# Kernel tuning notes

Measured on AMD Instinct MI355X. Metric: run time of the kernel, lower is better.

## Reference

```python
import jax, jax.numpy as jnp
import numpy as np

GRID_SIZE = 5
NUM_BASES = 2 ** GRID_SIZE - 1  # 31: actual number of Haar bases produced by the loop

def _haar_edges():
    left, mid, right = [], [], []
    for level in range(GRID_SIZE):
        scale = 2 ** level
        for shift in range(scale):
            left.append(shift / scale)
            mid.append((shift + 0.5) / scale)
            right.append((shift + 1.0) / scale)
    return (np.asarray(left, np.float32), np.asarray(mid, np.float32), np.asarray(right, np.float32))

_LEFT, _MID, _RIGHT = _haar_edges()


def setup_inputs() -> dict:
    key = jax.random.key(0)
    k1, k2, k3 = jax.random.split(key, 3)
    B, IN, OUT = 16384, 256, 256
    x = jax.random.normal(k1, (B, IN), dtype=jnp.float32)
    base_weight = jax.random.normal(k2, (OUT, IN), dtype=jnp.float32) * 0.05
    spline_weight = jax.random.normal(k3, (OUT, IN, NUM_BASES), dtype=jnp.float32) * 0.05
    spline_scaler = jnp.ones((OUT, IN), dtype=jnp.float32)
    return {"x": x, "base_weight": base_weight, "spline_weight": spline_weight, "spline_scaler": spline_scaler}


def reference(x, base_weight, spline_weight, spline_scaler):
    # per-feature min/max normalization over the batch dim
    x_min = jnp.min(x, axis=0, keepdims=True)
    x_max = jnp.max(x, axis=0, keepdims=True)
    xn = (x - x_min) / (x_max - x_min + 1e-8)            # [B, IN]
    left = jnp.asarray(_LEFT, x.dtype)
    mid = jnp.asarray(_MID, x.dtype)
    right = jnp.asarray(_RIGHT, x.dtype)
    xe = xn[..., None]                                    # [B, IN, 1]
    mask1 = ((xe >= left) & (xe < mid)).astype(x.dtype)
    mask2 = ((xe >= mid) & (xe < right)).astype(x.dtype)
    bases = mask1 - mask2                                 # [B, IN, NB]
    base_out = jax.nn.relu(x) @ base_weight.T             # [B, OUT]
    sw = spline_weight * spline_scaler[..., None]         # [OUT, IN, NB]
    wavelet_out = jnp.einsum('bik,oik->bo', bases, sw)    # [B, OUT]
    return base_out + wavelet_out
```

## Files before the change

kernel.cpp:

```cpp
#include <hip/hip_runtime.h>
#include <stdint.h>

typedef short s16x8 __attribute__((ext_vector_type(8)));
typedef float f32x4 __attribute__((ext_vector_type(4)));
typedef unsigned long long u64;

#define IN_F   256
#define OUT_F  256
#define BATCH  16384
#define NB     31
#define KONE   8192
#define KTOT   8448

typedef const __attribute__((address_space(1))) void* as1cvp;
typedef __attribute__((address_space(3))) void* as3vp;

__device__ __forceinline__ unsigned short f2bf(float f) {
    unsigned u = __float_as_uint(f);
    u += 0x7FFFu + ((u >> 16) & 1u);
    return (unsigned short)(u >> 16);
}

__global__ void minmax_part(const float* __restrict__ x,
                            float* __restrict__ pmn, float* __restrict__ pmx) {
    const int t = threadIdx.x;
    const int b0 = blockIdx.x * 32;
    float mn = 3.4e38f, mx = -3.4e38f;
    for (int r = 0; r < 32; ++r) {
        float v = x[(size_t)(b0 + r) * IN_F + t];
        mn = fminf(mn, v);
        mx = fmaxf(mx, v);
    }
    pmn[blockIdx.x * 256 + t] = mn;
    pmx[blockIdx.x * 256 + t] = mx;
}

__global__ __launch_bounds__(64) void minmax_reduce(
    const float* __restrict__ pmn, const float* __restrict__ pmx,
    float* __restrict__ xminF, float* __restrict__ rdenF) {
    const int j = blockIdx.x;
    const int lane = threadIdx.x;
    float mn = 3.4e38f, mx = -3.4e38f;
#pragma unroll
    for (int i = 0; i < 8; ++i) {
        int b = lane * 8 + i;
        mn = fminf(mn, pmn[(size_t)b * 256 + j]);
        mx = fmaxf(mx, pmx[(size_t)b * 256 + j]);
    }
#pragma unroll
    for (int off = 32; off; off >>= 1) {
        mn = fminf(mn, __shfl_down(mn, off));
        mx = fmaxf(mx, __shfl_down(mx, off));
    }
    if (lane == 0) {
        xminF[j] = mn;
        rdenF[j] = 1.0f / (mx - mn + 1e-8f);
    }
}

__global__ __launch_bounds__(256) void build_wb(
    const float* __restrict__ bw, const float* __restrict__ sw,
    const float* __restrict__ sc, unsigned short* __restrict__ Wb) {
    const int o = blockIdx.x, i = threadIdx.x;
    const float s = sc[o * IN_F + i];
    const float* swp = sw + (size_t)(o * IN_F + i) * NB;
    float w[NB];
#pragma unroll
    for (int k = 0; k < NB; ++k) w[k] = swp[k];
    unsigned short* dst = Wb + (size_t)o * KTOT + i * 32;
#pragma unroll
    for (int q = 0; q < 4; ++q) {
        union { s16x8 v; unsigned short s8[8]; } pk;
#pragma unroll
        for (int e = 0; e < 8; ++e) {
            int j = q * 8 + e;
            float acc = 0.f;
#pragma unroll
            for (int l = 0; l < 5; ++l) {
                int kk = (1 << l) - 1 + (j >> (5 - l));
                acc += (((j >> (4 - l)) & 1) ? -w[kk] : w[kk]);
            }
            pk.s8[e] = f2bf(acc * s);
        }
        *(s16x8*)(dst + q * 8) = pk.v;
    }
    Wb[(size_t)o * KTOT + KONE + i] = f2bf(bw[o * IN_F + i]);
}

__global__ __launch_bounds__(256) void leafk(
    const float* __restrict__ x, const float* __restrict__ xminF,
    const float* __restrict__ rdenF, unsigned char* __restrict__ lt) {
    const int lane = threadIdx.x & 63, w = threadIdx.x >> 6;
    const int b0 = blockIdx.x * 64;
    const float4 mn = *(const float4*)(xminF + lane * 4);
    const float4 rd = *(const float4*)(rdenF + lane * 4);
#pragma unroll 4
    for (int r = 0; r < 16; ++r) {
        int row = b0 + w * 16 + r;
        float4 v = *(const float4*)(x + (size_t)row * IN_F + lane * 4);
        unsigned b[4];
        float xs[4] = {v.x, v.y, v.z, v.w};
        float ms[4] = {mn.x, mn.y, mn.z, mn.w};
        float rs[4] = {rd.x, rd.y, rd.z, rd.w};
#pragma unroll
        for (int e = 0; e < 4; ++e) {
            float xn = (xs[e] - ms[e]) * rs[e];
            int l = (int)(xn * 32.0f);
            b[e] = (l >= 0 && l < 32) ? (unsigned)l : 255u;
        }
        unsigned pk = b[0] | (b[1] << 8) | (b[2] << 16) | (b[3] << 24);
        *(unsigned*)(lt + (size_t)row * IN_F + lane * 4) = pk;
    }
}

__global__ __launch_bounds__(256, 4) void gemm_kan(
    const float* __restrict__ x,
    const unsigned short* __restrict__ Wb,
    const unsigned char* __restrict__ lt,
    float* __restrict__ out)
{
    __shared__ unsigned short Bsh[2 * 64 * 64];

    const int t    = threadIdx.x;
    const int lane = t & 63;
    const int wv   = t >> 6;

    const int bid   = blockIdx.x;
    const int sid   = (bid & 7) * 128 + (bid >> 3);
    const int mtile = sid & 127;
    const int ntile = (sid >> 7) & 3;
    const int zz    = sid >> 9;
    const int kbeg  = zz ? 68 : 0;
    const int kend  = zz ? 132 : 68;

    const unsigned char* bbase = (const unsigned char*)(Wb
        + (size_t)(ntile * 64 + wv * 16 + (lane >> 3)) * KTOT
        + (((lane & 7) ^ (lane >> 3)) << 3));

    const int rr = lane & 15, kq = lane >> 4;
    const int r0 = mtile * 128 + wv * 32 + rr;
    const unsigned char* lp0 = lt + (size_t)r0 * IN_F;
    const unsigned char* lp1 = lt + (size_t)(r0 + 16) * IN_F;

    int boff[2][4];
#pragma unroll
    for (int ks = 0; ks < 2; ++ks)
#pragma unroll
        for (int nt = 0; nt < 4; ++nt) {
            int n = nt * 16 + rr, c = ks * 4 + kq;
            boff[ks][nt] = (n << 7) + ((c ^ (n & 7)) << 4);
        }

    {
        const unsigned char* src = bbase + (size_t)kbeg * 128;
        unsigned short* dst = Bsh + (kbeg & 1) * 4096 + wv * 1024;
#pragma unroll
        for (int qq = 0; qq < 2; ++qq)
            __builtin_amdgcn_global_load_lds(
                (as1cvp)(src + (size_t)qq * 8 * KTOT * 2),
                (as3vp)(uint32_t)(uintptr_t)(dst + qq * 512), 16, 0, 0);
    }
    u64 L0 = *(const u64*)(lp0 + 2 * kbeg);
    u64 L1 = *(const u64*)(lp1 + 2 * kbeg);
    __syncthreads();

    f32x4 acc[2][4] = {};

    for (int kb0 = kbeg; kb0 < kend; kb0 += 4) {
        u64 nL0 = L0, nL1 = L1;
        if (kb0 + 4 < kend && kb0 + 4 < 128) {
            nL0 = *(const u64*)(lp0 + 2 * (kb0 + 4));
            nL1 = *(const u64*)(lp1 + 2 * (kb0 + 4));
        }
        const bool denseg = (kb0 >= 128);
#pragma unroll
        for (int j = 0; j < 4; ++j) {
            const int kb = kb0 + j;
            const int cur = kb & 1;

            if (kb + 1 < kend) {
                const unsigned char* src = bbase + (size_t)(kb + 1) * 128;
                unsigned short* dst = Bsh + (1 - cur) * 4096 + wv * 1024;
#pragma unroll
                for (int qq = 0; qq < 2; ++qq)
                    __builtin_amdgcn_global_load_lds(
                        (as1cvp)(src + (size_t)qq * 8 * KTOT * 2),
                        (as3vp)(uint32_t)(uintptr_t)(dst + qq * 512), 16, 0, 0);
            }

            s16x8 af[2][2];
            if (!denseg) {
#pragma unroll
                for (int ks = 0; ks < 2; ++ks)
#pragma unroll
                    for (int mt = 0; mt < 2; ++mt) {
                        const u64 Lw = mt ? L1 : L0;
                        const int L = (int)((Lw >> (((j << 1) | ks) << 3)) & 255u);
                        unsigned hot = ((L >> 3) == kq) ? (0x3F80u << ((L & 1) << 4)) : 0u;
                        int slot = (L >> 1) & 3;
                        union { s16x8 v; unsigned u[4]; } a;
                        a.u[0] = (slot == 0) ? hot : 0u;
                        a.u[1] = (slot == 1) ? hot : 0u;
                        a.u[2] = (slot == 2) ? hot : 0u;
                        a.u[3] = (slot == 3) ? hot : 0u;
                        af[ks][mt] = a.v;
                    }
            } else {
#pragma unroll
                for (int ks = 0; ks < 2; ++ks)
#pragma unroll
                    for (int mt = 0; mt < 2; ++mt) {
                        const float* xr = x + (size_t)(r0 + mt * 16) * IN_F
                                            + (kb - 128) * 64 + ks * 32 + kq * 8;
                        union { s16x8 v; unsigned short s8[8]; } a;
#pragma unroll
                        for (int e = 0; e < 8; ++e) a.s8[e] = f2bf(fmaxf(xr[e], 0.0f));
                        af[ks][mt] = a.v;
                    }
            }

            const char* bb = (const char*)Bsh + cur * 8192;
#pragma unroll
            for (int ks = 0; ks < 2; ++ks) {
                s16x8 bfr[4];
#pragma unroll
                for (int nt = 0; nt < 4; ++nt)
                    bfr[nt] = *(const s16x8*)(bb + boff[ks][nt]);
#pragma unroll
                for (int mt = 0; mt < 2; ++mt)
#pragma unroll
                    for (int nt = 0; nt < 4; ++nt)
                        acc[mt][nt] = __builtin_amdgcn_mfma_f32_16x16x32_bf16(
                            af[ks][mt], bfr[nt], acc[mt][nt], 0, 0, 0);
            }
            __syncthreads();
        }
        L0 = nL0; L1 = nL1;
    }

    const int rq = lane >> 4;
#pragma unroll
    for (int mt = 0; mt < 2; ++mt)
#pragma unroll
        for (int nt = 0; nt < 4; ++nt)
#pragma unroll
            for (int v = 0; v < 4; ++v) {
                int row = mtile * 128 + wv * 32 + mt * 16 + rq * 4 + v;
                int col = ntile * 64 + nt * 16 + rr;
                atomicAdd(&out[(size_t)row * OUT_F + col], acc[mt][nt][v]);
            }
}

extern "C" void kernel_launch(void* const* d_in, const int* in_sizes, int n_in,
                              void* d_out, int out_size, void* d_ws, size_t ws_size,
                              hipStream_t stream) {
    (void)in_sizes; (void)n_in; (void)out_size; (void)ws_size;
    const float* x  = (const float*)d_in[0];
    const float* bw = (const float*)d_in[1];
    const float* sw = (const float*)d_in[2];
    const float* sc = (const float*)d_in[3];
    float* out = (float*)d_out;

    char* ws = (char*)d_ws;
    unsigned short* Wb   = (unsigned short*)ws;
    unsigned char*  lt   = (unsigned char*)(ws + 4325376);
    float* pmn   = (float*)(ws + 4325376);
    float* pmx   = (float*)(ws + 4325376 + 524288);
    float* xminF = (float*)(ws + 8519680);
    float* rdenF = (float*)(ws + 8520704);

    hipMemsetAsync(out, 0, (size_t)BATCH * OUT_F * 4, stream);

    minmax_part<<<512, 256, 0, stream>>>(x, pmn, pmx);
    minmax_reduce<<<256, 64, 0, stream>>>(pmn, pmx, xminF, rdenF);
    build_wb<<<256, 256, 0, stream>>>(bw, sw, sc, Wb);
    leafk<<<256, 256, 0, stream>>>(x, xminF, rdenF, lt);
    gemm_kan<<<1024, 256, 0, stream>>>(x, Wb, lt, out);
}
```

Baseline: 175.6 us.

## Fuse prep kernels with output zeroing; give each wave private B staging in GEMM

```diff
diff --git a/kernel.cpp b/kernel.cpp
--- a/kernel.cpp
+++ b/kernel.cpp
@@ -21,18 +21,52 @@
     return (unsigned short)(u >> 16);
 }
 
-__global__ void minmax_part(const float* __restrict__ x,
-                            float* __restrict__ pmn, float* __restrict__ pmx) {
-    const int t = threadIdx.x;
-    const int b0 = blockIdx.x * 32;
-    float mn = 3.4e38f, mx = -3.4e38f;
-    for (int r = 0; r < 32; ++r) {
-        float v = x[(size_t)(b0 + r) * IN_F + t];
-        mn = fminf(mn, v);
-        mx = fmaxf(mx, v);
-    }
-    pmn[blockIdx.x * 256 + t] = mn;
-    pmx[blockIdx.x * 256 + t] = mx;
+__global__ __launch_bounds__(256) void prep1(
+    const float* __restrict__ x, const float* __restrict__ bw,
+    const float* __restrict__ sw, const float* __restrict__ sc,
+    float* __restrict__ pmn, float* __restrict__ pmx,
+    unsigned short* __restrict__ Wb, float* __restrict__ outz) {
+    const int blk = blockIdx.x, t = threadIdx.x;
+    if (blk < 512) {
+        float4 z; z.x = z.y = z.z = z.w = 0.f;
+        float4* oz = (float4*)outz + (size_t)blk * 2048;
+#pragma unroll
+        for (int r = 0; r < 8; ++r) oz[t + r * 256] = z;
+        const int b0 = blk * 32;
+        float mn = 3.4e38f, mx = -3.4e38f;
+        for (int r = 0; r < 32; ++r) {
+            float v = x[(size_t)(b0 + r) * IN_F + t];
+            mn = fminf(mn, v);
+            mx = fmaxf(mx, v);
+        }
+        pmn[blk * 256 + t] = mn;
+        pmx[blk * 256 + t] = mx;
+    } else {
+        const int o = blk - 512, i = t;
+        const float s = sc[o * IN_F + i];
+        const float* swp = sw + (size_t)(o * IN_F + i) * NB;
+        float w[NB];
+#pragma unroll
+        for (int k = 0; k < NB; ++k) w[k] = swp[k];
+        unsigned short* dst = Wb + (size_t)o * KTOT + i * 32;
+#pragma unroll
+        for (int q = 0; q < 4; ++q) {
+            union { s16x8 v; unsigned short s8[8]; } pk;
+#pragma unroll
+            for (int e = 0; e < 8; ++e) {
+                int j = q * 8 + e;
+                float acc = 0.f;
+#pragma unroll
+                for (int l = 0; l < 5; ++l) {
+                    int kk = (1 << l) - 1 + (j >> (5 - l));
+                    acc += (((j >> (4 - l)) & 1) ? -w[kk] : w[kk]);
+                }
+                pk.s8[e] = f2bf(acc * s);
+            }
+            *(s16x8*)(dst + q * 8) = pk.v;
+        }
+        Wb[(size_t)o * KTOT + KONE + i] = f2bf(bw[o * IN_F + i]);
+    }
 }
 
 __global__ __launch_bounds__(64) void minmax_reduce(
@@ -56,35 +90,6 @@
         xminF[j] = mn;
         rdenF[j] = 1.0f / (mx - mn + 1e-8f);
     }
-}
-
-__global__ __launch_bounds__(256) void build_wb(
-    const float* __restrict__ bw, const float* __restrict__ sw,
-    const float* __restrict__ sc, unsigned short* __restrict__ Wb) {
-    const int o = blockIdx.x, i = threadIdx.x;
-    const float s = sc[o * IN_F + i];
-    const float* swp = sw + (size_t)(o * IN_F + i) * NB;
-    float w[NB];
-#pragma unroll
-    for (int k = 0; k < NB; ++k) w[k] = swp[k];
-    unsigned short* dst = Wb + (size_t)o * KTOT + i * 32;
-#pragma unroll
-    for (int q = 0; q < 4; ++q) {
-        union { s16x8 v; unsigned short s8[8]; } pk;
-#pragma unroll
-        for (int e = 0; e < 8; ++e) {
-            int j = q * 8 + e;
-            float acc = 0.f;
-#pragma unroll
-            for (int l = 0; l < 5; ++l) {
-                int kk = (1 << l) - 1 + (j >> (5 - l));
-                acc += (((j >> (4 - l)) & 1) ? -w[kk] : w[kk]);
-            }
-            pk.s8[e] = f2bf(acc * s);
-        }
-        *(s16x8*)(dst + q * 8) = pk.v;
-    }
-    Wb[(size_t)o * KTOT + KONE + i] = f2bf(bw[o * IN_F + i]);
 }
 
 __global__ __launch_bounds__(256) void leafk(
@@ -119,11 +124,12 @@
     const unsigned char* __restrict__ lt,
     float* __restrict__ out)
 {
-    __shared__ unsigned short Bsh[2 * 64 * 64];
+    __shared__ unsigned short Bsh[4][2][2048];
 
     const int t    = threadIdx.x;
     const int lane = t & 63;
     const int wv   = t >> 6;
+    const int wm   = wv & 1, wn = wv >> 1;
 
     const int bid   = blockIdx.x;
     const int sid   = (bid & 7) * 128 + (bid >> 3);
@@ -133,68 +139,82 @@
     const int kbeg  = zz ? 68 : 0;
     const int kend  = zz ? 132 : 68;
 
+    const int rr = lane & 15, kq = lane >> 4;
+    const int mbase = mtile * 128 + wm * 64;
+    const int nb    = ntile * 64 + wn * 32;
+
     const unsigned char* bbase = (const unsigned char*)(Wb
-        + (size_t)(ntile * 64 + wv * 16 + (lane >> 3)) * KTOT
-        + (((lane & 7) ^ (lane >> 3)) << 3));
-
-    const int rr = lane & 15, kq = lane >> 4;
-    const int r0 = mtile * 128 + wv * 32 + rr;
-    const unsigned char* lp0 = lt + (size_t)r0 * IN_F;
-    const unsigned char* lp1 = lt + (size_t)(r0 + 16) * IN_F;
-
-    int boff[2][4];
+        + (size_t)(nb + (lane >> 3)) * KTOT + (((lane & 7) ^ (lane >> 3)) << 3));
+
+    const unsigned char* lp0 = lt + (size_t)(mbase +  0 + rr) * IN_F;
+    const unsigned char* lp1 = lt + (size_t)(mbase + 16 + rr) * IN_F;
+    const unsigned char* lp2 = lt + (size_t)(mbase + 32 + rr) * IN_F;
+    const unsigned char* lp3 = lt + (size_t)(mbase + 48 + rr) * IN_F;
+
+    int boff[2][2];
 #pragma unroll
     for (int ks = 0; ks < 2; ++ks)
 #pragma unroll
-        for (int nt = 0; nt < 4; ++nt) {
-            int n = nt * 16 + rr, c = ks * 4 + kq;
-            boff[ks][nt] = (n << 7) + ((c ^ (n & 7)) << 4);
-        }
-
-    {
-        const unsigned char* src = bbase + (size_t)kbeg * 128;
-        unsigned short* dst = Bsh + (kbeg & 1) * 4096 + wv * 1024;
-#pragma unroll
-        for (int qq = 0; qq < 2; ++qq)
-            __builtin_amdgcn_global_load_lds(
-                (as1cvp)(src + (size_t)qq * 8 * KTOT * 2),
-                (as3vp)(uint32_t)(uintptr_t)(dst + qq * 512), 16, 0, 0);
-    }
+        for (int nt = 0; nt < 2; ++nt) {
+            int nn = nt * 16 + rr, c = ks * 4 + kq;
+            boff[ks][nt] = (nn << 7) + ((c ^ (nn & 7)) << 4);
+        }
+    const char* bufb[2] = { (const char*)&Bsh[wv][0][0], (const char*)&Bsh[wv][1][0] };
+
+#define STAGE(KB)                                                              \
+    {                                                                          \
+        const unsigned char* _src = bbase + (size_t)(KB) * 128;                \
+        unsigned short* _dst = &Bsh[wv][(KB) & 1][0];                          \
+        _Pragma("unroll")                                                      \
+        for (int q = 0; q < 4; ++q)                                            \
+            __builtin_amdgcn_global_load_lds(                                  \
+                (as1cvp)(_src + (size_t)q * 8 * KTOT * 2),                     \
+                (as3vp)(uint32_t)(uintptr_t)(_dst + q * 512), 16, 0, 0);       \
+    }
+
     u64 L0 = *(const u64*)(lp0 + 2 * kbeg);
     u64 L1 = *(const u64*)(lp1 + 2 * kbeg);
-    __syncthreads();
-
-    f32x4 acc[2][4] = {};
+    u64 L2 = *(const u64*)(lp2 + 2 * kbeg);
+    u64 L3 = *(const u64*)(lp3 + 2 * kbeg);
+    STAGE(kbeg);
+
+    f32x4 acc[4][2] = {};
 
     for (int kb0 = kbeg; kb0 < kend; kb0 += 4) {
-        u64 nL0 = L0, nL1 = L1;
+        u64 nL0 = L0, nL1 = L1, nL2 = L2, nL3 = L3;
         if (kb0 + 4 < kend && kb0 + 4 < 128) {
             nL0 = *(const u64*)(lp0 + 2 * (kb0 + 4));
             nL1 = *(const u64*)(lp1 + 2 * (kb0 + 4));
+            nL2 = *(const u64*)(lp2 + 2 * (kb0 + 4));
+            nL3 = *(const u64*)(lp3 + 2 * (kb0 + 4));
+            asm volatile("" : "+v"(nL0), "+v"(nL1), "+v"(nL2), "+v"(nL3));
         }
         const bool denseg = (kb0 >= 128);
 #pragma unroll
         for (int j = 0; j < 4; ++j) {
             const int kb = kb0 + j;
-            const int cur = kb & 1;
-
             if (kb + 1 < kend) {
-                const unsigned char* src = bbase + (size_t)(kb + 1) * 128;
-                unsigned short* dst = Bsh + (1 - cur) * 4096 + wv * 1024;
-#pragma unroll
-                for (int qq = 0; qq < 2; ++qq)
-                    __builtin_amdgcn_global_load_lds(
-                        (as1cvp)(src + (size_t)qq * 8 * KTOT * 2),
-                        (as3vp)(uint32_t)(uintptr_t)(dst + qq * 512), 16, 0, 0);
-            }
-
-            s16x8 af[2][2];
+                STAGE(kb + 1);
+                asm volatile("s_waitcnt vmcnt(4)" ::: "memory");
+            } else {
+                asm volatile("s_waitcnt vmcnt(0)" ::: "memory");
+            }
+
+            const char* bb = bufb[kb & 1];
+            s16x8 bfr[2][2];
+#pragma unroll
+            for (int ks = 0; ks < 2; ++ks)
+#pragma unroll
+                for (int nt = 0; nt < 2; ++nt)
+                    bfr[ks][nt] = *(const s16x8*)(bb + boff[ks][nt]);
+
+            s16x8 af[2][4];
             if (!denseg) {
 #pragma unroll
                 for (int ks = 0; ks < 2; ++ks)
 #pragma unroll
-                    for (int mt = 0; mt < 2; ++mt) {
-                        const u64 Lw = mt ? L1 : L0;
+                    for (int mt = 0; mt < 4; ++mt) {
+                        const u64 Lw = (mt == 0) ? L0 : (mt == 1) ? L1 : (mt == 2) ? L2 : L3;
                         const int L = (int)((Lw >> (((j << 1) | ks) << 3)) & 255u);
                         unsigned hot = ((L >> 3) == kq) ? (0x3F80u << ((L & 1) << 4)) : 0u;
                         int slot = (L >> 1) & 3;
@@ -209,8 +229,8 @@
 #pragma unroll
                 for (int ks = 0; ks < 2; ++ks)
 #pragma unroll
-                    for (int mt = 0; mt < 2; ++mt) {
-                        const float* xr = x + (size_t)(r0 + mt * 16) * IN_F
+                    for (int mt = 0; mt < 4; ++mt) {
+                        const float* xr = x + (size_t)(mbase + mt * 16 + rr) * IN_F
                                             + (kb - 128) * 64 + ks * 32 + kq * 8;
                         union { s16x8 v; unsigned short s8[8]; } a;
 #pragma unroll
@@ -219,36 +239,32 @@
                     }
             }
 
-            const char* bb = (const char*)Bsh + cur * 8192;
-#pragma unroll
-            for (int ks = 0; ks < 2; ++ks) {
-                s16x8 bfr[4];
-#pragma unroll
-                for (int nt = 0; nt < 4; ++nt)
-                    bfr[nt] = *(const s16x8*)(bb + boff[ks][nt]);
-#pragma unroll
-                for (int mt = 0; mt < 2; ++mt)
-#pragma unroll
-                    for (int nt = 0; nt < 4; ++nt)
+            __builtin_amdgcn_s_setprio(1);
+#pragma unroll
+            for (int ks = 0; ks < 2; ++ks)
+#pragma unroll
+                for (int mt = 0; mt < 4; ++mt)
+#pragma unroll
+                    for (int nt = 0; nt < 2; ++nt)
                         acc[mt][nt] = __builtin_amdgcn_mfma_f32_16x16x32_bf16(
-                            af[ks][mt], bfr[nt], acc[mt][nt], 0, 0, 0);
-            }
-            __syncthreads();
-        }
-        L0 = nL0; L1 = nL1;
+                            af[ks][mt], bfr[ks][nt], acc[mt][nt], 0, 0, 0);
+            __builtin_amdgcn_s_setprio(0);
+        }
+        L0 = nL0; L1 = nL1; L2 = nL2; L3 = nL3;
     }
 
     const int rq = lane >> 4;
 #pragma unroll
-    for (int mt = 0; mt < 2; ++mt)
-#pragma unroll
-        for (int nt = 0; nt < 4; ++nt)
+    for (int mt = 0; mt < 4; ++mt)
+#pragma unroll
+        for (int nt = 0; nt < 2; ++nt)
 #pragma unroll
             for (int v = 0; v < 4; ++v) {
-                int row = mtile * 128 + wv * 32 + mt * 16 + rq * 4 + v;
-                int col = ntile * 64 + nt * 16 + rr;
+                int row = mbase + mt * 16 + rq * 4 + v;
+                int col = nb + nt * 16 + rr;
                 atomicAdd(&out[(size_t)row * OUT_F + col], acc[mt][nt][v]);
             }
+#undef STAGE
 }
 
 extern "C" void kernel_launch(void* const* d_in, const int* in_sizes, int n_in,
@@ -269,11 +285,8 @@
     float* xminF = (float*)(ws + 8519680);
     float* rdenF = (float*)(ws + 8520704);
 
-    hipMemsetAsync(out, 0, (size_t)BATCH * OUT_F * 4, stream);
-
-    minmax_part<<<512, 256, 0, stream>>>(x, pmn, pmx);
+    prep1<<<768, 256, 0, stream>>>(x, bw, sw, sc, pmn, pmx, Wb, out);
     minmax_reduce<<<256, 64, 0, stream>>>(pmn, pmx, xminF, rdenF);
-    build_wb<<<256, 256, 0, stream>>>(bw, sw, sc, Wb);
     leafk<<<256, 256, 0, stream>>>(x, xminF, rdenF, lt);
     gemm_kan<<<1024, 256, 0, stream>>>(x, Wb, lt, out);
 }
```

New measurement: 207.4 us. 18.1% more time.
